# Optimization experiments

Hardware: AMD Instinct MI355X
Metric: run time of the kernel (lower is better)

The kernel has to match this reference:

```python
import jax, jax.numpy as jnp
import numpy as np

B, T, N, NFG, NFR = 16, 16, 512, 128, 64
OW = 80.0  # cfg.out_size[1]
POS_THRESHOLD = 0.2  # cfg.pos_threshold


def setup_inputs() -> dict:
    key = jax.random.key(0)
    ks = jax.random.split(key, 7)
    graph_boxes_features = jax.random.normal(ks[0], (B, T, N, NFG), dtype=jnp.float32)
    # box corners (x1,y1,x2,y2) in image coordinates [0, OW)
    boxes_in_flat = jax.random.uniform(ks[1], (B * T * N, 4), dtype=jnp.float32) * OW
    W = jax.random.normal(ks[2], (NFG, NFG), dtype=jnp.float32) * 0.02
    theta_w = jax.random.normal(ks[3], (NFR, NFG), dtype=jnp.float32) * 0.05
    theta_b = jax.random.normal(ks[4], (NFR,), dtype=jnp.float32) * 0.01
    phi_w = jax.random.normal(ks[5], (NFR, NFG), dtype=jnp.float32) * 0.05
    phi_b = jax.random.normal(ks[6], (NFR,), dtype=jnp.float32) * 0.01
    return {
        "graph_boxes_features": graph_boxes_features,
        "boxes_in_flat": boxes_in_flat,
        "W": W,
        "theta_w": theta_w,
        "theta_b": theta_b,
        "phi_w": phi_w,
        "phi_b": phi_b,
    }


def reference(graph_boxes_features, boxes_in_flat, W, theta_w, theta_b, phi_w, phi_b):
    b, t, n, nfg = graph_boxes_features.shape
    nfr = theta_w.shape[0]

    # box centers -> pairwise Euclidean distances per (b,t) frame
    cx = (boxes_in_flat[:, 0] + boxes_in_flat[:, 2]) * 0.5
    cy = (boxes_in_flat[:, 1] + boxes_in_flat[:, 3]) * 0.5
    pos = jnp.stack([cx, cy], axis=-1).reshape(b * t, n, 2)  # [BT, N, 2]
    diff = pos[:, :, None, :] - pos[:, None, :, :]           # [BT, N, N, 2]
    dist = jnp.sqrt(jnp.sum(diff * diff, axis=-1))           # [BT, N, N]
    position_mask = (dist > POS_THRESHOLD * OW).reshape(b, t, n, n)

    # relation graph: scaled QK^T with distance masking, softmax over last N
    theta = jnp.einsum("btnf,rf->btnr", graph_boxes_features, theta_w) + theta_b
    phi = jnp.einsum("btnf,rf->btnr", graph_boxes_features, phi_w) + phi_b
    sim = jnp.einsum("btnr,btmr->btnm", theta, phi) / np.float32(np.sqrt(nfr))
    sim = jnp.where(position_mask, -jnp.inf, sim)
    relation_graph = jax.nn.softmax(sim, axis=-1)            # [B, T, N, N]

    # neighbor aggregation + output projection
    n2npool = jnp.einsum("btnm,btmf->btnf", relation_graph, graph_boxes_features)
    out = jnp.einsum("btnf,fg->btng", n2npool, W)            # [B, T, N, NFG]
    return out, relation_graph
```

## Files before the change

### kernel.cpp

```cpp
#include <hip/hip_runtime.h>
#include <hip/hip_bf16.h>

#define NN 512
#define NFG 128
#define NFR 64
#define BT 256

typedef __attribute__((ext_vector_type(8))) short bfrag;
typedef __attribute__((ext_vector_type(4))) float f32x4;

__device__ __forceinline__ short f2bf(float f) {
    unsigned u = __float_as_uint(f);
    return (short)((u + 0x7fffu + ((u >> 16) & 1u)) >> 16);
}
__device__ __forceinline__ float bf2f(short s) {
    return __uint_as_float(((unsigned)(unsigned short)s) << 16);
}

__global__ __launch_bounds__(256) void k_prep(const float* __restrict__ W,
                                              short* __restrict__ WtB) {
    int i = blockIdx.x * 256 + threadIdx.x;
    if (i < NFG * NFG) { int f = i >> 7, g = i & 127; WtB[g * NFG + f] = f2bf(W[i]); }
}

__global__ __launch_bounds__(256) void k_projF(const float* __restrict__ X,
                                               const float* __restrict__ thw,
                                               const float* __restrict__ thb,
                                               const float* __restrict__ phw,
                                               const float* __restrict__ phb,
                                               const short* __restrict__ WtB,
                                               short* __restrict__ thetaS,
                                               short* __restrict__ phiX,
                                               short* __restrict__ YtG) {
    __shared__ short Xs[64][136];
    __shared__ short wS[2][64][136];
    __shared__ float bS[2][64];
    const int bt = blockIdx.y, bx = blockIdx.x, n0 = bx * 64, tid = threadIdx.x;

    {
        int row = tid >> 2, seg = tid & 3;
        const float* src = X + ((size_t)(bt * NN + n0 + row)) * NFG + seg * 32;
        short tmp[32];
        #pragma unroll
        for (int k = 0; k < 8; ++k) {
            float4 v = reinterpret_cast<const float4*>(src)[k];
            tmp[k*4+0] = f2bf(v.x); tmp[k*4+1] = f2bf(v.y);
            tmp[k*4+2] = f2bf(v.z); tmp[k*4+3] = f2bf(v.w);
        }
        #pragma unroll
        for (int k = 0; k < 4; ++k)
            reinterpret_cast<uint4*>(&Xs[row][seg * 32])[k] =
                reinterpret_cast<uint4*>(tmp)[k];
    }
    #pragma unroll
    for (int k = 0; k < 32; ++k) {
        int idx = k * 256 + tid;
        int r = idx >> 7, f = idx & 127;
        wS[0][r][f] = f2bf(thw[idx]);
        wS[1][r][f] = f2bf(phw[idx]);
    }
    if (tid < 64) { bS[0][tid] = thb[tid]; bS[1][tid] = phb[tid]; }
    __syncthreads();

    const int wid = tid >> 6, lane = tid & 63;
    const int l16 = lane & 15, lg = lane >> 4;

    bfrag xa[4];
    #pragma unroll
    for (int kk = 0; kk < 4; ++kk)
        xa[kk] = *reinterpret_cast<const bfrag*>(&Xs[wid * 16 + l16][kk * 32 + lg * 8]);

    for (int pass = 0; pass < 2; ++pass) {
        const float sc = pass ? 1.0f : 0.125f;
        #pragma unroll
        for (int c = 0; c < 4; ++c) {
            f32x4 acc = {0.f, 0.f, 0.f, 0.f};
            #pragma unroll
            for (int kk = 0; kk < 4; ++kk) {
                bfrag b = *reinterpret_cast<const bfrag*>(
                    &wS[pass][c * 16 + l16][kk * 32 + lg * 8]);
                acc = __builtin_amdgcn_mfma_f32_16x16x32_bf16(xa[kk], b, acc, 0, 0, 0);
            }
            float bv = bS[pass][c * 16 + l16];
            if (pass == 0) {
                #pragma unroll
                for (int r = 0; r < 4; ++r) {
                    int n = n0 + wid * 16 + lg * 4 + r;
                    thetaS[((size_t)(bt * NN + n)) * NFR + c * 16 + l16] =
                        f2bf((acc[r] + bv) * sc);
                }
            } else {
                const size_t tbase = (size_t)bt * (NN * NFR)
                                   + (size_t)(bx * 4 + wid) * 1024
                                   + (c >> 1) * 512;
                const int lgp = (c & 1) * 2 + (l16 >> 3);
                const int e = l16 & 7;
                #pragma unroll
                for (int r = 0; r < 4; ++r) {
                    phiX[tbase + (size_t)(lgp * 16 + lg * 4 + r) * 8 + e] =
                        f2bf(acc[r] + bv);
                }
            }
        }
    }

    const size_t ybase = (size_t)bt * NFG * NN;
    #pragma unroll
    for (int gi = 0; gi < 2; ++gi) {
        int gs = wid * 2 + gi;
        bfrag wa[4];
        #pragma unroll
        for (int kk = 0; kk < 4; ++kk)
            wa[kk] = *reinterpret_cast<const bfrag*>(
                &WtB[(gs * 16 + l16) * NFG + kk * 32 + lg * 8]);
        #pragma unroll
        for (int ms = 0; ms < 4; ++ms) {
            f32x4 acc = {0.f, 0.f, 0.f, 0.f};
            #pragma unroll
            for (int kk = 0; kk < 4; ++kk) {
                bfrag xb = *reinterpret_cast<const bfrag*>(
                    &Xs[ms * 16 + l16][kk * 32 + lg * 8]);
                acc = __builtin_amdgcn_mfma_f32_16x16x32_bf16(wa[kk], xb, acc, 0, 0, 0);
            }
            #pragma unroll
            for (int r = 0; r < 4; ++r) {
                int g = gs * 16 + lg * 4 + r;
                int m = n0 + ms * 16 + l16;
                YtG[ybase + (size_t)((m >> 5) * NFG + g) * 32 + (m & 31)] = f2bf(acc[r]);
            }
        }
    }
}

__global__ __launch_bounds__(128, 4) void k_fused4(const short* __restrict__ thetaS,
                                                   const short* __restrict__ phiX,
                                                   const short* __restrict__ YtG,
                                                   const float* __restrict__ boxes,
                                                   float* __restrict__ outG,
                                                   float* __restrict__ rgG) {
    __shared__ short S[16 * 512];
    __shared__ float2 c2s[NN];
    __shared__ float partS[2][16];
    const int bid = blockIdx.x;
    const int jj = bid >> 3;
    const int bt = (bid & 7) * 32 + (jj >> 5);
    const int n0 = (jj & 31) * 16;
    const int tid = threadIdx.x;
    const int wid = tid >> 6, lane = tid & 63;
    const int l16 = lane & 15, lg = lane >> 4;
    const int r8 = l16 & 7;
    const size_t fr = (size_t)bt * NN;
    const float THR = __uint_as_float(0x43800001u);

    {
        #pragma unroll
        for (int k = 0; k < 4; ++k) {
            int row = k * 128 + tid;
            float4 b = reinterpret_cast<const float4*>(boxes)[fr + row];
            c2s[row] = make_float2(__fmul_rn(__fadd_rn(b.x, b.z), 0.5f),
                                   __fmul_rn(__fadd_rn(b.y, b.w), 0.5f));
        }
    }

    bfrag thB0 = *reinterpret_cast<const bfrag*>(&thetaS[(fr + n0 + l16) * NFR + lg * 8]);
    bfrag thB1 = *reinterpret_cast<const bfrag*>(&thetaS[(fr + n0 + l16) * NFR + 32 + lg * 8]);
    __syncthreads();

    const float2 cn = c2s[n0 + l16];

    const short* pXf = phiX + (size_t)bt * (NN * NFR)
                     + (size_t)wid * 16 * 1024 + lane * 8;
    bfrag pf0[4], pf1[4];
    #pragma unroll
    for (int t = 0; t < 4; ++t) {
        pf0[t] = *reinterpret_cast<const bfrag*>(pXf + t * 1024);
        pf1[t] = *reinterpret_cast<const bfrag*>(pXf + t * 1024 + 512);
    }
    float smv = 0.f;
    #pragma unroll
    for (int t = 0; t < 16; ++t) {
        bfrag pa0 = pf0[t & 3], pa1 = pf1[t & 3];
        if (t + 4 < 16) {
            pf0[t & 3] = *reinterpret_cast<const bfrag*>(pXf + (t + 4) * 1024);
            pf1[t & 3] = *reinterpret_cast<const bfrag*>(pXf + (t + 4) * 1024 + 512);
        }
        const int mb = wid * 256 + t * 16;
        f32x4 acc = {0.f, 0.f, 0.f, 0.f};
        __builtin_amdgcn_s_setprio(1);
        acc = __builtin_amdgcn_mfma_f32_16x16x32_bf16(pa0, thB0, acc, 0, 0, 0);
        acc = __builtin_amdgcn_mfma_f32_16x16x32_bf16(pa1, thB1, acc, 0, 0, 0);
        __builtin_amdgcn_s_setprio(0);
        float e[4];
        #pragma unroll
        for (int r = 0; r < 4; ++r) {
            int m = mb + lg * 4 + r;
            float2 cm = c2s[m];
            float dx = __fsub_rn(cn.x, cm.x), dy = __fsub_rn(cn.y, cm.y);
            float d2 = __fadd_rn(__fmul_rn(dx, dx), __fmul_rn(dy, dy));
            e[r] = (d2 > THR) ? 0.f : __expf(acc[r]);
        }
        smv += (e[0] + e[1]) + (e[2] + e[3]);
        unsigned q0, q1;
        asm("v_cvt_pk_bf16_f32 %0, %1, %2" : "=v"(q0) : "v"(e[0]), "v"(e[1]));
        asm("v_cvt_pk_bf16_f32 %0, %1, %2" : "=v"(q1) : "v"(e[2]), "v"(e[3]));
        uint2 qq; qq.x = q0; qq.y = q1;
        const int g = wid * 32 + t * 2 + (lg >> 1);
        *reinterpret_cast<uint2*>(
            &S[(l16 << 9) + ((g ^ r8) << 3) + ((lg & 1) << 2)]) = qq;
    }
    smv += __shfl_xor(smv, 16);
    smv += __shfl_xor(smv, 32);
    if (lane < 16) partS[wid][l16] = smv;
    __syncthreads();

    const float inv = 1.0f / (partS[0][l16] + partS[1][l16]);

    f32x4 pool[4];
    #pragma unroll
    for (int gi = 0; gi < 4; ++gi) pool[gi] = f32x4{0.f, 0.f, 0.f, 0.f};
    const short* ybp = YtG + (size_t)bt * NFG * NN
                     + wid * 2048 + l16 * 32 + lg * 8;
    float* rp = rgG + (fr + n0 + l16) * NN;

    bfrag yb[2][4];
    #pragma unroll
    for (int gi = 0; gi < 4; ++gi)
        yb[0][gi] = *reinterpret_cast<const bfrag*>(ybp + gi * 512);
    bfrag pa = *reinterpret_cast<const bfrag*>(&S[(l16 << 9) + ((lg ^ r8) << 3)]);

    #pragma unroll
    for (int c = 0; c < 16; ++c) {
        if (c + 1 < 16) {
            #pragma unroll
            for (int gi = 0; gi < 4; ++gi)
                yb[(c + 1) & 1][gi] = *reinterpret_cast<const bfrag*>(
                    ybp + (c + 1) * 4096 + gi * 512);
        }
        bfrag pa_cur = pa;
        if (c + 1 < 16)
            pa = *reinterpret_cast<const bfrag*>(
                &S[(l16 << 9) + ((((c + 1) * 4 + lg) ^ r8) << 3)]);
        __builtin_amdgcn_s_setprio(1);
        #pragma unroll
        for (int gi = 0; gi < 4; ++gi)
            pool[gi] = __builtin_amdgcn_mfma_f32_16x16x32_bf16(
                pa_cur, yb[c & 1][gi], pool[gi], 0, 0, 0);
        __builtin_amdgcn_s_setprio(0);
        if (wid == (c >> 3)) {
            f32x4 aa, bb;
            aa[0] = bf2f(pa_cur[0]) * inv; aa[1] = bf2f(pa_cur[1]) * inv;
            aa[2] = bf2f(pa_cur[2]) * inv; aa[3] = bf2f(pa_cur[3]) * inv;
            bb[0] = bf2f(pa_cur[4]) * inv; bb[1] = bf2f(pa_cur[5]) * inv;
            bb[2] = bf2f(pa_cur[6]) * inv; bb[3] = bf2f(pa_cur[7]) * inv;
            __builtin_nontemporal_store(aa,
                reinterpret_cast<f32x4*>(rp + c * 32 + lg * 8));
            __builtin_nontemporal_store(bb,
                reinterpret_cast<f32x4*>(rp + c * 32 + lg * 8 + 4));
        }
    }

    float iv[4];
    #pragma unroll
    for (int r = 0; r < 4; ++r)
        iv[r] = 1.0f / (partS[0][lg * 4 + r] + partS[1][lg * 4 + r]);
    #pragma unroll
    for (int gi = 0; gi < 4; ++gi) {
        #pragma unroll
        for (int r = 0; r < 4; ++r) {
            __builtin_nontemporal_store(pool[gi][r] * iv[r],
                &outG[(fr + n0 + lg * 4 + r) * NFG + wid * 64 + gi * 16 + l16]);
        }
    }
}

__global__ __launch_bounds__(256) void k_proj(const float* __restrict__ X,
                                              const float* __restrict__ thw,
                                              const float* __restrict__ thb,
                                              const float* __restrict__ phw,
                                              const float* __restrict__ phb,
                                              short* __restrict__ thetaS,
                                              short* __restrict__ phiS) {
    __shared__ short Xs[64][136];
    __shared__ short wS[2][64][136];
    __shared__ float bS[2][64];
    const int bt = blockIdx.y, n0 = blockIdx.x * 64, tid = threadIdx.x;
    {
        int row = tid >> 2, seg = tid & 3;
        const float* src = X + ((size_t)(bt * NN + n0 + row)) * NFG + seg * 32;
        short tmp[32];
        #pragma unroll
        for (int k = 0; k < 8; ++k) {
            float4 v = reinterpret_cast<const float4*>(src)[k];
            tmp[k*4+0] = f2bf(v.x); tmp[k*4+1] = f2bf(v.y);
            tmp[k*4+2] = f2bf(v.z); tmp[k*4+3] = f2bf(v.w);
        }
        #pragma unroll
        for (int k = 0; k < 4; ++k)
            reinterpret_cast<uint4*>(&Xs[row][seg * 32])[k] =
                reinterpret_cast<uint4*>(tmp)[k];
    }
    #pragma unroll
    for (int k = 0; k < 32; ++k) {
        int idx = k * 256 + tid;
        int r = idx >> 7, f = idx & 127;
        wS[0][r][f] = f2bf(thw[idx]);
        wS[1][r][f] = f2bf(phw[idx]);
    }
    if (tid < 64) { bS[0][tid] = thb[tid]; bS[1][tid] = phb[tid]; }
    __syncthreads();
    const int wid = tid >> 6, lane = tid & 63;
    const int l16 = lane & 15, lg = lane >> 4;
    bfrag xa[4];
    #pragma unroll
    for (int kk = 0; kk < 4; ++kk)
        xa[kk] = *reinterpret_cast<const bfrag*>(&Xs[wid * 16 + l16][kk * 32 + lg * 8]);
    for (int pass = 0; pass < 2; ++pass) {
        short* dst = pass ? phiS : thetaS;
        #pragma unroll
        for (int c = 0; c < 4; ++c) {
            f32x4 acc = {0.f, 0.f, 0.f, 0.f};
            #pragma unroll
            for (int kk = 0; kk < 4; ++kk) {
                bfrag b = *reinterpret_cast<const bfrag*>(
                    &wS[pass][c * 16 + l16][kk * 32 + lg * 8]);
                acc = __builtin_amdgcn_mfma_f32_16x16x32_bf16(xa[kk], b, acc, 0, 0, 0);
            }
            float bv = bS[pass][c * 16 + l16];
            #pragma unroll
            for (int r = 0; r < 4; ++r) {
                int n = n0 + wid * 16 + lg * 4 + r;
                dst[((size_t)(bt * NN + n)) * NFR + c * 16 + l16] = f2bf(acc[r] + bv);
            }
        }
    }
}

__global__ __launch_bounds__(512) void k_sim(const short* __restrict__ thetaS,
                                             const short* __restrict__ phiS,
                                             const float* __restrict__ boxes,
                                             float* __restrict__ rgG) {
    __shared__ float S[64][516];
    __shared__ float cxs[NN], cys[NN];
    const int bt = blockIdx.y, n0 = blockIdx.x * 64, tid = threadIdx.x;
    const int wid = tid >> 6, lane = tid & 63;
    const int l16 = lane & 15, lg = lane >> 4;
    const int rsub = wid & 3, ch = wid >> 2;
    {
        float4 b = reinterpret_cast<const float4*>(boxes)[bt * NN + tid];
        cxs[tid] = __fmul_rn(__fadd_rn(b.x, b.z), 0.5f);
        cys[tid] = __fmul_rn(__fadd_rn(b.y, b.w), 0.5f);
    }
    bfrag thA[2];
    #pragma unroll
    for (int kk = 0; kk < 2; ++kk)
        thA[kk] = *reinterpret_cast<const bfrag*>(
            &thetaS[((size_t)(bt * NN + n0 + rsub * 16 + l16)) * NFR + kk * 32 + lg * 8]);
    __syncthreads();
    #pragma unroll 1
    for (int mt = 0; mt < 8; ++mt) {
        int m0 = mt * 64;
        #pragma unroll
        for (int ci = 0; ci < 2; ++ci) {
            int cs = ch * 2 + ci;
            int m = m0 + cs * 16 + l16;
            f32x4 acc = {0.f, 0.f, 0.f, 0.f};
            #pragma unroll
            for (int kk = 0; kk < 2; ++kk) {
                bfrag pb = *reinterpret_cast<const bfrag*>(
                    &phiS[((size_t)(bt * NN + m)) * NFR + kk * 32 + lg * 8]);
                acc = __builtin_amdgcn_mfma_f32_16x16x32_bf16(thA[kk], pb, acc, 0, 0, 0);
            }
            float cxm = cxs[m], cym = cys[m];
            #pragma unroll
            for (int r = 0; r < 4; ++r) {
                int nl = rsub * 16 + lg * 4 + r;
                float dx = __fsub_rn(cxs[n0 + nl], cxm);
                float dy = __fsub_rn(cys[n0 + nl], cym);
                float d2 = __fadd_rn(__fmul_rn(dx, dx), __fmul_rn(dy, dy));
                S[nl][m] = (d2 > __uint_as_float(0x43800001u))
                               ? -__builtin_inff() : acc[r] * 0.125f;
            }
        }
    }
    __syncthreads();
    {
        int row = tid >> 3, j = tid & 7;
        float* Sp = &S[row][j * 64];
        float mx = -__builtin_inff();
        #pragma unroll
        for (int k = 0; k < 16; ++k) {
            float4 v = *reinterpret_cast<float4*>(Sp + k * 4);
            mx = fmaxf(mx, fmaxf(fmaxf(v.x, v.y), fmaxf(v.z, v.w)));
        }
        mx = fmaxf(mx, __shfl_xor(mx, 1));
        mx = fmaxf(mx, __shfl_xor(mx, 2));
        mx = fmaxf(mx, __shfl_xor(mx, 4));
        float sm = 0.f;
        #pragma unroll
        for (int k = 0; k < 16; ++k) {
            float4 v = *reinterpret_cast<float4*>(Sp + k * 4);
            v.x = __expf(v.x - mx); v.y = __expf(v.y - mx);
            v.z = __expf(v.z - mx); v.w = __expf(v.w - mx);
            sm += (v.x + v.y) + (v.z + v.w);
            *reinterpret_cast<float4*>(Sp + k * 4) = v;
        }
        sm += __shfl_xor(sm, 1);
        sm += __shfl_xor(sm, 2);
        sm += __shfl_xor(sm, 4);
        float inv = 1.0f / sm;
        float* rp = rgG + ((size_t)(bt * NN) + n0 + row) * NN + j * 64;
        #pragma unroll
        for (int k = 0; k < 16; ++k) {
            float4 a = *reinterpret_cast<float4*>(Sp + k * 4);
            a.x *= inv; a.y *= inv; a.z *= inv; a.w *= inv;
            *reinterpret_cast<float4*>(rp + k * 4) = a;
        }
    }
}

__global__ __launch_bounds__(256) void k_pool(const float* __restrict__ rgG,
                                              const float* __restrict__ X,
                                              const float* __restrict__ W,
                                              float* __restrict__ outG) {
    __shared__ short Xt[128][72];
    __shared__ short poolS[64][136];
    __shared__ short WtS[128][136];
    const int bt = blockIdx.y, n0 = blockIdx.x * 64, tid = threadIdx.x;
    const int wid = tid >> 6, lane = tid & 63;
    const int l16 = lane & 15, lg = lane >> 4;
    #pragma unroll
    for (int k = 0; k < 64; ++k) {
        int idx = k * 256 + tid;
        int f = idx >> 7, g = idx & 127;
        WtS[g][f] = f2bf(W[idx]);
    }
    f32x4 acc[8];
    #pragma unroll
    for (int ft = 0; ft < 8; ++ft) acc[ft] = f32x4{0.f, 0.f, 0.f, 0.f};
    #pragma unroll 1
    for (int mt = 0; mt < 8; ++mt) {
        __syncthreads();
        {
            int m = tid >> 2, seg = tid & 3;
            const float* src = X + ((size_t)(bt * NN + mt * 64 + m)) * NFG + seg * 32;
            #pragma unroll
            for (int k = 0; k < 8; ++k) {
                float4 v = reinterpret_cast<const float4*>(src)[k];
                int f = seg * 32 + k * 4;
                Xt[f + 0][m] = f2bf(v.x); Xt[f + 1][m] = f2bf(v.y);
                Xt[f + 2][m] = f2bf(v.z); Xt[f + 3][m] = f2bf(v.w);
            }
        }
        bfrag pa[2];
        const float* prow = rgG + ((size_t)(bt * NN + n0 + wid * 16 + l16)) * NN + mt * 64;
        #pragma unroll
        for (int kk = 0; kk < 2; ++kk) {
            float4 a = *reinterpret_cast<const float4*>(prow + kk * 32 + lg * 8);
            float4 b = *reinterpret_cast<const float4*>(prow + kk * 32 + lg * 8 + 4);
            short t[8] = { f2bf(a.x), f2bf(a.y), f2bf(a.z), f2bf(a.w),
                           f2bf(b.x), f2bf(b.y), f2bf(b.z), f2bf(b.w) };
            pa[kk] = *reinterpret_cast<bfrag*>(t);
        }
        __syncthreads();
        #pragma unroll
        for (int ft = 0; ft < 8; ++ft) {
            #pragma unroll
            for (int kk = 0; kk < 2; ++kk) {
                bfrag b = *reinterpret_cast<const bfrag*>(
                    &Xt[ft * 16 + l16][kk * 32 + lg * 8]);
                acc[ft] = __builtin_amdgcn_mfma_f32_16x16x32_bf16(pa[kk], b, acc[ft], 0, 0, 0);
            }
        }
    }
    __syncthreads();
    #pragma unroll
    for (int ft = 0; ft < 8; ++ft)
        #pragma unroll
        for (int r = 0; r < 4; ++r)
            poolS[wid * 16 + lg * 4 + r][ft * 16 + l16] = f2bf(acc[ft][r]);
    __syncthreads();
    bfrag a2[4];
    #pragma unroll
    for (int kk = 0; kk < 4; ++kk)
        a2[kk] = *reinterpret_cast<const bfrag*>(&poolS[wid * 16 + l16][kk * 32 + lg * 8]);
    #pragma unroll
    for (int gt = 0; gt < 8; ++gt) {
        f32x4 o = {0.f, 0.f, 0.f, 0.f};
        #pragma unroll
        for (int kk = 0; kk < 4; ++kk) {
            bfrag b2 = *reinterpret_cast<const bfrag*>(&WtS[gt * 16 + l16][kk * 32 + lg * 8]);
            o = __builtin_amdgcn_mfma_f32_16x16x32_bf16(a2[kk], b2, o, 0, 0, 0);
        }
        #pragma unroll
        for (int r = 0; r < 4; ++r) {
            int n = n0 + wid * 16 + lg * 4 + r;
            outG[((size_t)(bt * NN + n)) * NFG + gt * 16 + l16] = o[r];
        }
    }
}

extern "C" void kernel_launch(void* const* d_in, const int* in_sizes, int n_in,
                              void* d_out, int out_size, void* d_ws, size_t ws_size,
                              hipStream_t stream) {
    const float* X     = (const float*)d_in[0];
    const float* boxes = (const float*)d_in[1];
    const float* W     = (const float*)d_in[2];
    const float* thw   = (const float*)d_in[3];
    const float* thb   = (const float*)d_in[4];
    const float* phw   = (const float*)d_in[5];
    const float* phb   = (const float*)d_in[6];

    float* outR = (float*)d_out;
    float* rgR  = outR + (size_t)BT * NN * NFG;

    const size_t TH = (size_t)BT * NN * NFR * 2;
    const size_t YT = (size_t)BT * NFG * NN * 2;
    const size_t WS_NEED = TH * 2 + YT + (size_t)NFG * NFG * 2;
    if (ws_size >= WS_NEED) {
        char* ws = (char*)d_ws;
        short* thetaS = (short*)(ws);
        short* phiX   = (short*)(ws + TH);
        short* YtG    = (short*)(ws + 2 * TH);
        short* WtB    = (short*)(ws + 2 * TH + YT);
        k_prep  <<<64, 256, 0, stream>>>(W, WtB);
        k_projF <<<dim3(8, BT), 256, 0, stream>>>(X, thw, thb, phw, phb, WtB,
                                                  thetaS, phiX, YtG);
        k_fused4<<<8192, 128, 0, stream>>>(thetaS, phiX, YtG, boxes, outR, rgR);
    } else {
        short* thetaS = (short*)d_out;
        short* phiS   = thetaS + (size_t)BT * NN * NFR;
        k_proj<<<dim3(8, BT), 256, 0, stream>>>(X, thw, thb, phw, phb, thetaS, phiS);
        k_sim <<<dim3(8, BT), 512, 0, stream>>>(thetaS, phiS, boxes, rgR);
        k_pool<<<dim3(8, BT), 256, 0, stream>>>(rgR, X, W, outR);
    }
}
```

Measured before the change: 154.7 us.

## Process 32 query rows per block with four waves in fused relation kernel

```diff
diff --git a/kernel.cpp b/kernel.cpp
--- a/kernel.cpp
+++ b/kernel.cpp
@@ -132,44 +132,49 @@
     }
 }
 
-__global__ __launch_bounds__(128, 4) void k_fused4(const short* __restrict__ thetaS,
+__global__ __launch_bounds__(256, 4) void k_fused5(const short* __restrict__ thetaS,
                                                    const short* __restrict__ phiX,
                                                    const short* __restrict__ YtG,
                                                    const float* __restrict__ boxes,
                                                    float* __restrict__ outG,
                                                    float* __restrict__ rgG) {
-    __shared__ short S[16 * 512];
+    __shared__ short S[32 * 512];
     __shared__ float2 c2s[NN];
-    __shared__ float partS[2][16];
+    __shared__ float partS[2][32];
     const int bid = blockIdx.x;
     const int jj = bid >> 3;
-    const int bt = (bid & 7) * 32 + (jj >> 5);
-    const int n0 = (jj & 31) * 16;
+    const int bt = (bid & 7) * 32 + (jj >> 4);
+    const int n0 = (jj & 15) * 32;
     const int tid = threadIdx.x;
     const int wid = tid >> 6, lane = tid & 63;
     const int l16 = lane & 15, lg = lane >> 4;
+    const int ns = wid & 1;
+    const int mh = wid >> 1;
     const int r8 = l16 & 7;
+    const int nloc = ns * 16 + l16;
     const size_t fr = (size_t)bt * NN;
     const float THR = __uint_as_float(0x43800001u);
 
     {
         #pragma unroll
-        for (int k = 0; k < 4; ++k) {
-            int row = k * 128 + tid;
+        for (int k = 0; k < 2; ++k) {
+            int row = k * 256 + tid;
             float4 b = reinterpret_cast<const float4*>(boxes)[fr + row];
             c2s[row] = make_float2(__fmul_rn(__fadd_rn(b.x, b.z), 0.5f),
                                    __fmul_rn(__fadd_rn(b.y, b.w), 0.5f));
         }
     }
 
-    bfrag thB0 = *reinterpret_cast<const bfrag*>(&thetaS[(fr + n0 + l16) * NFR + lg * 8]);
-    bfrag thB1 = *reinterpret_cast<const bfrag*>(&thetaS[(fr + n0 + l16) * NFR + 32 + lg * 8]);
-    __syncthreads();
-
-    const float2 cn = c2s[n0 + l16];
+    bfrag thB0 = *reinterpret_cast<const bfrag*>(
+        &thetaS[(fr + n0 + nloc) * NFR + lg * 8]);
+    bfrag thB1 = *reinterpret_cast<const bfrag*>(
+        &thetaS[(fr + n0 + nloc) * NFR + 32 + lg * 8]);
+    __syncthreads();
+
+    const float2 cn = c2s[n0 + nloc];
 
     const short* pXf = phiX + (size_t)bt * (NN * NFR)
-                     + (size_t)wid * 16 * 1024 + lane * 8;
+                     + (size_t)mh * 16 * 1024 + lane * 8;
     bfrag pf0[4], pf1[4];
     #pragma unroll
     for (int t = 0; t < 4; ++t) {
@@ -184,7 +189,7 @@
             pf0[t & 3] = *reinterpret_cast<const bfrag*>(pXf + (t + 4) * 1024);
             pf1[t & 3] = *reinterpret_cast<const bfrag*>(pXf + (t + 4) * 1024 + 512);
         }
-        const int mb = wid * 256 + t * 16;
+        const int mb = mh * 256 + t * 16;
         f32x4 acc = {0.f, 0.f, 0.f, 0.f};
         __builtin_amdgcn_s_setprio(1);
         acc = __builtin_amdgcn_mfma_f32_16x16x32_bf16(pa0, thB0, acc, 0, 0, 0);
@@ -204,29 +209,29 @@
         asm("v_cvt_pk_bf16_f32 %0, %1, %2" : "=v"(q0) : "v"(e[0]), "v"(e[1]));
         asm("v_cvt_pk_bf16_f32 %0, %1, %2" : "=v"(q1) : "v"(e[2]), "v"(e[3]));
         uint2 qq; qq.x = q0; qq.y = q1;
-        const int g = wid * 32 + t * 2 + (lg >> 1);
+        const int g = mh * 32 + t * 2 + (lg >> 1);
         *reinterpret_cast<uint2*>(
-            &S[(l16 << 9) + ((g ^ r8) << 3) + ((lg & 1) << 2)]) = qq;
+            &S[(nloc << 9) + ((g ^ r8) << 3) + ((lg & 1) << 2)]) = qq;
     }
     smv += __shfl_xor(smv, 16);
     smv += __shfl_xor(smv, 32);
-    if (lane < 16) partS[wid][l16] = smv;
-    __syncthreads();
-
-    const float inv = 1.0f / (partS[0][l16] + partS[1][l16]);
+    if (lane < 16) partS[mh][nloc] = smv;
+    __syncthreads();
+
+    const float inv = 1.0f / (partS[0][nloc] + partS[1][nloc]);
 
     f32x4 pool[4];
     #pragma unroll
     for (int gi = 0; gi < 4; ++gi) pool[gi] = f32x4{0.f, 0.f, 0.f, 0.f};
     const short* ybp = YtG + (size_t)bt * NFG * NN
-                     + wid * 2048 + l16 * 32 + lg * 8;
-    float* rp = rgG + (fr + n0 + l16) * NN;
+                     + mh * 2048 + l16 * 32 + lg * 8;
+    float* rp = rgG + (fr + n0 + nloc) * NN;
 
     bfrag yb[2][4];
     #pragma unroll
     for (int gi = 0; gi < 4; ++gi)
         yb[0][gi] = *reinterpret_cast<const bfrag*>(ybp + gi * 512);
-    bfrag pa = *reinterpret_cast<const bfrag*>(&S[(l16 << 9) + ((lg ^ r8) << 3)]);
+    bfrag pa = *reinterpret_cast<const bfrag*>(&S[(nloc << 9) + ((lg ^ r8) << 3)]);
 
     #pragma unroll
     for (int c = 0; c < 16; ++c) {
@@ -239,14 +244,14 @@
         bfrag pa_cur = pa;
         if (c + 1 < 16)
             pa = *reinterpret_cast<const bfrag*>(
-                &S[(l16 << 9) + ((((c + 1) * 4 + lg) ^ r8) << 3)]);
+                &S[(nloc << 9) + ((((c + 1) * 4 + lg) ^ r8) << 3)]);
         __builtin_amdgcn_s_setprio(1);
         #pragma unroll
         for (int gi = 0; gi < 4; ++gi)
             pool[gi] = __builtin_amdgcn_mfma_f32_16x16x32_bf16(
                 pa_cur, yb[c & 1][gi], pool[gi], 0, 0, 0);
         __builtin_amdgcn_s_setprio(0);
-        if (wid == (c >> 3)) {
+        if (mh == (c >> 3)) {
             f32x4 aa, bb;
             aa[0] = bf2f(pa_cur[0]) * inv; aa[1] = bf2f(pa_cur[1]) * inv;
             aa[2] = bf2f(pa_cur[2]) * inv; aa[3] = bf2f(pa_cur[3]) * inv;
@@ -262,13 +267,13 @@
     float iv[4];
     #pragma unroll
     for (int r = 0; r < 4; ++r)
-        iv[r] = 1.0f / (partS[0][lg * 4 + r] + partS[1][lg * 4 + r]);
+        iv[r] = 1.0f / (partS[0][ns * 16 + lg * 4 + r] + partS[1][ns * 16 + lg * 4 + r]);
     #pragma unroll
     for (int gi = 0; gi < 4; ++gi) {
         #pragma unroll
         for (int r = 0; r < 4; ++r) {
             __builtin_nontemporal_store(pool[gi][r] * iv[r],
-                &outG[(fr + n0 + lg * 4 + r) * NFG + wid * 64 + gi * 16 + l16]);
+                &outG[(fr + n0 + ns * 16 + lg * 4 + r) * NFG + mh * 64 + gi * 16 + l16]);
         }
     }
 }
@@ -525,7 +530,7 @@
         k_prep  <<<64, 256, 0, stream>>>(W, WtB);
         k_projF <<<dim3(8, BT), 256, 0, stream>>>(X, thw, thb, phw, phb, WtB,
                                                   thetaS, phiX, YtG);
-        k_fused4<<<8192, 128, 0, stream>>>(thetaS, phiX, YtG, boxes, outR, rgR);
+        k_fused5<<<4096, 256, 0, stream>>>(thetaS, phiX, YtG, boxes, outR, rgR);
     } else {
         short* thetaS = (short*)d_out;
         short* phiS   = thetaS + (size_t)BT * NN * NFR;
```

Result: no change. 153.0 us, median of 2 (-1.1%).
